# Performance work log

Hardware: AMD Instinct MI355X
Metric: run time of the kernel (lower is better)

## Reference

```python
import jax, jax.numpy as jnp
import numpy as np

B, L, D = 8, 4096, 512  # batch, seq_len (power of 2), in_features
R_MIN, R_MAX = 0.9, 0.999


def setup_inputs() -> dict:
    key = jax.random.key(0)
    k1, k2, k3 = jax.random.split(key, 3)
    inputs = jax.random.normal(k1, (B, L, D), dtype=jnp.float32)
    # Linear layers: i_dense D->2D, o_dense 2D->D (torch Linear: y = x @ W.T + b)
    Wi = jax.random.normal(k2, (2 * D, D), dtype=jnp.float32) / np.sqrt(D)
    bi = jnp.zeros((2 * D,), dtype=jnp.float32)
    Wo = jax.random.normal(k3, (D, 2 * D), dtype=jnp.float32) / np.sqrt(2 * D)
    bo = jnp.zeros((D,), dtype=jnp.float32)
    # LRU param init, exactly as in the torch module
    rng = np.random.RandomState(0)
    u1 = rng.random_sample(D)
    u2 = rng.random_sample(D)
    v_log = np.log(-0.5 * np.log(u1 * (R_MAX ** 2 - R_MIN ** 2) + R_MIN ** 2))
    theta_log = np.log(u2 * np.pi * 2)
    gamma_log = np.log(np.sqrt(1 - np.exp(-np.exp(v_log)) ** 2))
    params_log = jnp.asarray(np.stack([v_log, theta_log, gamma_log]), dtype=jnp.float32)
    return {"inputs": inputs, "Wi": Wi, "bi": bi, "Wo": Wo, "bo": bo,
            "params_log": params_log}


def reference(inputs, Wi, bi, Wo, bo, params_log):
    b, lin, d = inputs.shape
    u = inputs @ Wi.T + bi                       # [B, L, 2D]
    params = jnp.exp(params_log)                 # [3, D]
    v, theta, gamma = params[0], params[1], params[2]
    log2_L = int(np.ceil(np.log2(lin)))
    Lp = 2 ** log2_L
    # interleaved (real, imag) pairs -> complex state
    u = u.reshape(b, lin, d, 2)
    x = jax.lax.complex(u[..., 0], u[..., 1])    # [B, L, D] complex64
    if Lp > lin:
        x = jnp.pad(x, ((0, 0), (0, Lp - lin), (0, 0)))
    # Blelloch-style doubling scan: after stage i, each block of length 2^i
    # holds the prefix-scanned values x_t = lam*x_{t-1} + u_t within the block.
    for i in range(1, log2_L + 1):
        l = 2 ** i
        xr = x.reshape(b * Lp // l, l, d)
        x1, x2 = xr[:, : l // 2], xr[:, l // 2 :]
        pos = jnp.arange(1, l // 2 + 1, dtype=jnp.float32)        # [l/2]
        lambs = jnp.exp(jax.lax.complex(-pos[:, None] * v,
                                        pos[:, None] * theta))   # [l/2, D]
        x2 = x2 + lambs * x1[:, -1:]
        x = jnp.concatenate([x1, x2], axis=1).reshape(b, Lp, d)
    x = x[:, :lin] * gamma.astype(jnp.complex64)
    xr = jnp.concatenate([jnp.real(x), jnp.imag(x)], axis=-1)     # [B, L, 2D]
    out = xr @ Wo.T + bo
    return jax.nn.relu(out)
```

## Files before the change

kernel.cpp:

```cpp
#include <hip/hip_runtime.h>
#include <cstdint>
#include <cstddef>

typedef unsigned short u16;
typedef unsigned int   u32;

typedef short bf16x8 __attribute__((ext_vector_type(8)));
typedef float f32x4  __attribute__((ext_vector_type(4)));

__device__ __forceinline__ u16 f2bf(float f) {
  u32 u = __float_as_uint(f);
  u += 0x7fffu + ((u >> 16) & 1u);
  return (u16)(u >> 16);
}
__device__ __forceinline__ float bflo(u32 w) { return __uint_as_float((w & 0xffffu) << 16); }
__device__ __forceinline__ float bfhi(u32 w) { return __uint_as_float(w & 0xffff0000u); }

#define GLB_AS(p) ((const __attribute__((address_space(1))) void*)(p))
#define LDS_AS(p) ((__attribute__((address_space(3))) void*)(p))

__global__ __launch_bounds__(256)
void conv3_f32_bf16(const float* __restrict__ in, u16* __restrict__ a,
                    const float* __restrict__ wi, u16* __restrict__ wib,
                    const float* __restrict__ wo, u16* __restrict__ wob)
{
  long i = (long)blockIdx.x * 256 + threadIdx.x;
  const float* src; u16* dst;
  if (i < 4194304L) { src = in; dst = a; }
  else if (i < 4325376L) { i -= 4194304L; src = wi; dst = wib; }
  else { i -= 4325376L; if (i >= 131072L) return; src = wo; dst = wob; }
  float4 v = ((const float4*)src)[i];
  u32 lo = (u32)f2bf(v.x) | ((u32)f2bf(v.y) << 16);
  u32 hi = (u32)f2bf(v.z) | ((u32)f2bf(v.w) << 16);
  ((uint2*)dst)[i] = make_uint2(lo, hi);
}

template<int N, int K, int LOGNB, int OUT_BF16, int RELU>
__global__ __launch_bounds__(512, 4)
void gemm_w2(const u16* __restrict__ A, const u16* __restrict__ Bw,
             const float* __restrict__ bias, void* __restrict__ Cout)
{
  __shared__ __align__(16) u16 As[256 * 32];
  __shared__ __align__(16) u16 Bs[128 * 32];

  const int tid  = threadIdx.x;
  const int lane = tid & 63;
  const int wave = tid >> 6;
  const int bid  = blockIdx.x;
  const int xcd  = bid & 7;
  const int s    = bid >> 3;
  const int m0 = (xcd * 16 + (s >> LOGNB)) * 256;
  const int n0 = (s & ((1 << LOGNB) - 1)) * 128;
  const int wm = (wave & 3) * 64;
  const int wn = (wave >> 2) * 64;

  f32x4 acc[4][4];
#pragma unroll
  for (int i = 0; i < 4; ++i)
#pragma unroll
    for (int j = 0; j < 4; ++j) acc[i][j] = f32x4{0.f, 0.f, 0.f, 0.f};

  const u16* Ap[2]; const u16* Bp; int ldsA[2]; int ldsB;
#pragma unroll
  for (int i = 0; i < 2; ++i) {
    int g = i * 512 + tid;
    int r = g >> 2;
    int koff = ((g & 3) ^ ((r >> 1) & 3)) << 3;
    Ap[i]   = A + (size_t)(m0 + r) * K + koff;
    ldsA[i] = (i * 512 + wave * 64) * 8;
  }
  {
    int g = tid;
    int r = g >> 2;
    int koff = ((g & 3) ^ ((r >> 1) & 3)) << 3;
    Bp   = Bw + (size_t)(n0 + r) * K + koff;
    ldsB = (wave * 64) * 8;
  }

  const int fm = lane & 15;
  const int q  = lane >> 4;
  int aoff[4], boff[4];
#pragma unroll
  for (int i = 0; i < 4; ++i) {
    int m = wm + i * 16 + fm;
    aoff[i] = (m * 4 + (q ^ ((m >> 1) & 3))) * 8;
    int n = wn + i * 16 + fm;
    boff[i] = (n * 4 + (q ^ ((n >> 1) & 3))) * 8;
  }

  for (int kt = 0; kt < K; kt += 32) {
    __builtin_amdgcn_global_load_lds(GLB_AS(Ap[0] + kt), LDS_AS(As + ldsA[0]), 16, 0, 0);
    __builtin_amdgcn_global_load_lds(GLB_AS(Ap[1] + kt), LDS_AS(As + ldsA[1]), 16, 0, 0);
    __builtin_amdgcn_global_load_lds(GLB_AS(Bp    + kt), LDS_AS(Bs + ldsB),    16, 0, 0);
    __syncthreads();

    bf16x8 af[4], bf[4];
#pragma unroll
    for (int i = 0; i < 4; ++i) { af[i] = *(const bf16x8*)&As[aoff[i]];
                                  bf[i] = *(const bf16x8*)&Bs[boff[i]]; }
#pragma unroll
    for (int mi = 0; mi < 4; ++mi)
#pragma unroll
      for (int ni = 0; ni < 4; ++ni)
        acc[mi][ni] = __builtin_amdgcn_mfma_f32_16x16x32_bf16(af[mi], bf[ni],
                                                              acc[mi][ni], 0, 0, 0);
    __syncthreads();
  }

  const int colL = lane & 15;
  const int rowQ = (lane >> 4) * 4;
#pragma unroll
  for (int mi = 0; mi < 4; ++mi) {
#pragma unroll
    for (int ni = 0; ni < 4; ++ni) {
      int col  = n0 + wn + ni * 16 + colL;
      int rowb = m0 + wm + mi * 16 + rowQ;
      float bv = bias[col];
#pragma unroll
      for (int r = 0; r < 4; ++r) {
        float v = acc[mi][ni][r] + bv;
        if (RELU) v = fmaxf(v, 0.f);
        size_t idx = (size_t)(rowb + r) * N + col;
        if (OUT_BF16) ((u16*)Cout)[idx] = f2bf(v);
        else          ((float*)Cout)[idx] = v;
      }
    }
  }
}

__global__ __launch_bounds__(256)
void scan_chunk_end(const u16* __restrict__ u, const float* __restrict__ plog,
                    float2* __restrict__ e)
{
  const int t = threadIdx.x;
  const int c = blockIdx.x;
  const int b = blockIdx.y;
  const int j0 = 2 * t;
  float v0 = expf(plog[j0]),        v1 = expf(plog[j0 + 1]);
  float t0 = expf(plog[512 + j0]),  t1 = expf(plog[512 + j0 + 1]);
  float m0 = expf(-v0), m1 = expf(-v1);
  float lr0 = m0 * cosf(t0), li0 = m0 * sinf(t0);
  float lr1 = m1 * cosf(t1), li1 = m1 * sinf(t1);
  const uint2* up = (const uint2*)u;
  size_t idx = (size_t)(b * 4096 + c * 32) * 256 + t;
  float h0r = 0.f, h0i = 0.f, h1r = 0.f, h1i = 0.f;
#pragma unroll 8
  for (int s = 0; s < 32; ++s) {
    uint2 w = up[idx]; idx += 256;
    float u0r = bflo(w.x), u0i = bfhi(w.x);
    float u1r = bflo(w.y), u1i = bfhi(w.y);
    float n0r = fmaf(lr0, h0r, fmaf(-li0, h0i, u0r));
    float n0i = fmaf(lr0, h0i, fmaf( li0, h0r, u0i));
    float n1r = fmaf(lr1, h1r, fmaf(-li1, h1i, u1r));
    float n1i = fmaf(lr1, h1i, fmaf( li1, h1r, u1i));
    h0r = n0r; h0i = n0i; h1r = n1r; h1i = n1i;
  }
  ((float4*)e)[(size_t)(b * 128 + c) * 256 + t] = make_float4(h0r, h0i, h1r, h1i);
}

__global__ __launch_bounds__(256)
void scan_out2(const u16* __restrict__ u, const float* __restrict__ plog,
               const float2* __restrict__ e, u16* __restrict__ xr)
{
  const int t = threadIdx.x;
  const int c = blockIdx.x;
  const int b = blockIdx.y;
  const int j0 = 2 * t;
  float v0 = expf(plog[j0]),        v1 = expf(plog[j0 + 1]);
  float t0 = expf(plog[512 + j0]),  t1 = expf(plog[512 + j0 + 1]);
  float g0 = expf(plog[1024 + j0]), g1 = expf(plog[1024 + j0 + 1]);
  float m0 = expf(-v0), m1 = expf(-v1);
  float lr0 = m0 * cosf(t0), li0 = m0 * sinf(t0);
  float lr1 = m1 * cosf(t1), li1 = m1 * sinf(t1);

  float Lm0 = expf(-32.f * v0), Lm1 = expf(-32.f * v1);
  float La0 = 32.f * t0,        La1 = 32.f * t1;
  float Lr0 = Lm0 * cosf(La0), Li0 = Lm0 * sinf(La0);
  float Lr1 = Lm1 * cosf(La1), Li1 = Lm1 * sinf(La1);
  float h0r = 0.f, h0i = 0.f, h1r = 0.f, h1i = 0.f;
  const float4* e4 = (const float4*)e;
#pragma unroll 4
  for (int i = 0; i < c; ++i) {
    float4 ec = e4[(size_t)(b * 128 + i) * 256 + t];
    float n0r = fmaf(Lr0, h0r, fmaf(-Li0, h0i, ec.x));
    float n0i = fmaf(Lr0, h0i, fmaf( Li0, h0r, ec.y));
    float n1r = fmaf(Lr1, h1r, fmaf(-Li1, h1i, ec.z));
    float n1i = fmaf(Lr1, h1i, fmaf( Li1, h1r, ec.w));
    h0r = n0r; h0i = n0i; h1r = n1r; h1i = n1i;
  }

  const uint2* up = (const uint2*)u;
  u32* xp = (u32*)xr;
  size_t uidx = (size_t)(b * 4096 + c * 32) * 256 + t;
  size_t xidx = (size_t)(b * 4096 + c * 32) * 512 + t;
#pragma unroll 8
  for (int s = 0; s < 32; ++s) {
    uint2 w = up[uidx]; uidx += 256;
    float u0r = bflo(w.x), u0i = bfhi(w.x);
    float u1r = bflo(w.y), u1i = bfhi(w.y);
    float n0r = fmaf(lr0, h0r, fmaf(-li0, h0i, u0r));
    float n0i = fmaf(lr0, h0i, fmaf( li0, h0r, u0i));
    float n1r = fmaf(lr1, h1r, fmaf(-li1, h1i, u1r));
    float n1i = fmaf(lr1, h1i, fmaf( li1, h1r, u1i));
    h0r = n0r; h0i = n0i; h1r = n1r; h1i = n1i;
    xp[xidx]       = (u32)f2bf(g0 * h0r) | ((u32)f2bf(g1 * h1r) << 16);
    xp[xidx + 256] = (u32)f2bf(g0 * h0i) | ((u32)f2bf(g1 * h1i) << 16);
    xidx += 512;
  }
}

extern "C" void kernel_launch(void* const* d_in, const int* in_sizes, int n_in,
                              void* d_out, int out_size, void* d_ws, size_t ws_size,
                              hipStream_t stream)
{
  (void)in_sizes; (void)n_in; (void)out_size; (void)ws_size;
  const float* inputs = (const float*)d_in[0];
  const float* Wi     = (const float*)d_in[1];
  const float* bi     = (const float*)d_in[2];
  const float* Wo     = (const float*)d_in[3];
  const float* bo     = (const float*)d_in[4];
  const float* plog   = (const float*)d_in[5];

  char* ws = (char*)d_ws;
  u16*    xrA   = (u16*)(ws);
  u16*    u_bf  = (u16*)(ws + 67108864ull);
  u16*    Wi_bf = (u16*)(ws + 134217728ull);
  u16*    Wo_bf = (u16*)(ws + 135266304ull);
  float2* e_b   = (float2*)(ws + 136314880ull);

  conv3_f32_bf16<<<17408, 256, 0, stream>>>(inputs, xrA, Wi, Wi_bf, Wo, Wo_bf);

  gemm_w2<1024, 512, 3, 1, 0><<<1024, 512, 0, stream>>>(xrA, Wi_bf, bi, u_bf);

  scan_chunk_end<<<dim3(128, 8), 256, 0, stream>>>(u_bf, plog, e_b);
  scan_out2<<<dim3(128, 8), 256, 0, stream>>>(u_bf, plog, e_b, xrA);

  gemm_w2<512, 1024, 2, 0, 1><<<512, 512, 0, stream>>>(xrA, Wo_bf, bo, d_out);
}
```

Before: 258.6 us.

## Triple-buffer GEMM LDS loads and add a separate chunk-carry scan kernel

The GEMM main loop now uses three LDS buffers with global_load_lds prefetch two tiles ahead, so the second barrier per k-step goes away and loads overlap the MFMA work. The scan's cross-chunk carry moves into a new 8-block kernel that sequentially propagates the chunk-end states in place. Before, each scan_out2 block re-scanned every earlier chunk, which is quadratic redundant work. The plog parameter loads are also vectorized. Costs are triple the GEMM LDS footprint, which may lower occupancy, plus an extra serial, low-parallelism kernel launch.

After: 252.5 us. -2.4%, faster.

```diff
diff --git a/kernel.cpp b/kernel.cpp
--- a/kernel.cpp
+++ b/kernel.cpp
@@ -40,8 +40,8 @@
 void gemm_w2(const u16* __restrict__ A, const u16* __restrict__ Bw,
              const float* __restrict__ bias, void* __restrict__ Cout)
 {
-  __shared__ __align__(16) u16 As[256 * 32];
-  __shared__ __align__(16) u16 Bs[128 * 32];
+  __shared__ __align__(16) u16 As[3][256 * 32];
+  __shared__ __align__(16) u16 Bs[3][128 * 32];
 
   const int tid  = threadIdx.x;
   const int lane = tid & 63;
@@ -88,24 +88,37 @@
     boff[i] = (n * 4 + (q ^ ((n >> 1) & 3))) * 8;
   }
 
-  for (int kt = 0; kt < K; kt += 32) {
-    __builtin_amdgcn_global_load_lds(GLB_AS(Ap[0] + kt), LDS_AS(As + ldsA[0]), 16, 0, 0);
-    __builtin_amdgcn_global_load_lds(GLB_AS(Ap[1] + kt), LDS_AS(As + ldsA[1]), 16, 0, 0);
-    __builtin_amdgcn_global_load_lds(GLB_AS(Bp    + kt), LDS_AS(Bs + ldsB),    16, 0, 0);
-    __syncthreads();
-
-    bf16x8 af[4], bf[4];
-#pragma unroll
-    for (int i = 0; i < 4; ++i) { af[i] = *(const bf16x8*)&As[aoff[i]];
-                                  bf[i] = *(const bf16x8*)&Bs[boff[i]]; }
+  auto stage = [&](int buf, int kt) {
+    __builtin_amdgcn_global_load_lds(GLB_AS(Ap[0] + kt), LDS_AS(&As[buf][ldsA[0]]), 16, 0, 0);
+    __builtin_amdgcn_global_load_lds(GLB_AS(Ap[1] + kt), LDS_AS(&As[buf][ldsA[1]]), 16, 0, 0);
+    __builtin_amdgcn_global_load_lds(GLB_AS(Bp    + kt), LDS_AS(&Bs[buf][ldsB]),    16, 0, 0);
+  };
+  auto compute = [&](int buf) {
+    bf16x8 af[4], bfr[4];
+#pragma unroll
+    for (int i = 0; i < 4; ++i) { af[i]  = *(const bf16x8*)&As[buf][aoff[i]];
+                                  bfr[i] = *(const bf16x8*)&Bs[buf][boff[i]]; }
 #pragma unroll
     for (int mi = 0; mi < 4; ++mi)
 #pragma unroll
       for (int ni = 0; ni < 4; ++ni)
-        acc[mi][ni] = __builtin_amdgcn_mfma_f32_16x16x32_bf16(af[mi], bf[ni],
+        acc[mi][ni] = __builtin_amdgcn_mfma_f32_16x16x32_bf16(af[mi], bfr[ni],
                                                               acc[mi][ni], 0, 0, 0);
-    __syncthreads();
-  }
+  };
+
+  constexpr int NT = K / 32;
+  stage(0, 0);
+  stage(1, 32);
+#pragma unroll
+  for (int t = 0; t < NT - 1; ++t) {
+    asm volatile("s_waitcnt vmcnt(3)" ::: "memory");
+    __builtin_amdgcn_s_barrier();
+    if (t + 2 < NT) stage((t + 2) % 3, (t + 2) * 32);
+    compute(t % 3);
+  }
+  asm volatile("s_waitcnt vmcnt(0)" ::: "memory");
+  __builtin_amdgcn_s_barrier();
+  compute((NT - 1) % 3);
 
   const int colL = lane & 15;
   const int rowQ = (lane >> 4) * 4;
@@ -135,9 +148,10 @@
   const int t = threadIdx.x;
   const int c = blockIdx.x;
   const int b = blockIdx.y;
-  const int j0 = 2 * t;
-  float v0 = expf(plog[j0]),        v1 = expf(plog[j0 + 1]);
-  float t0 = expf(plog[512 + j0]),  t1 = expf(plog[512 + j0 + 1]);
+  float2 vl = ((const float2*)plog)[t];
+  float2 tl = ((const float2*)plog)[256 + t];
+  float v0 = expf(vl.x), v1 = expf(vl.y);
+  float t0 = expf(tl.x), t1 = expf(tl.y);
   float m0 = expf(-v0), m1 = expf(-v1);
   float lr0 = m0 * cosf(t0), li0 = m0 * sinf(t0);
   float lr1 = m1 * cosf(t1), li1 = m1 * sinf(t1);
@@ -159,34 +173,53 @@
 }
 
 __global__ __launch_bounds__(256)
-void scan_out2(const u16* __restrict__ u, const float* __restrict__ plog,
-               const float2* __restrict__ e, u16* __restrict__ xr)
+void scan_mid(const float* __restrict__ plog, float4* __restrict__ e)
 {
   const int t = threadIdx.x;
-  const int c = blockIdx.x;
-  const int b = blockIdx.y;
-  const int j0 = 2 * t;
-  float v0 = expf(plog[j0]),        v1 = expf(plog[j0 + 1]);
-  float t0 = expf(plog[512 + j0]),  t1 = expf(plog[512 + j0 + 1]);
-  float g0 = expf(plog[1024 + j0]), g1 = expf(plog[1024 + j0 + 1]);
-  float m0 = expf(-v0), m1 = expf(-v1);
-  float lr0 = m0 * cosf(t0), li0 = m0 * sinf(t0);
-  float lr1 = m1 * cosf(t1), li1 = m1 * sinf(t1);
-
+  const int b = blockIdx.x;
+  float2 vl = ((const float2*)plog)[t];
+  float2 tl = ((const float2*)plog)[256 + t];
+  float v0 = expf(vl.x), v1 = expf(vl.y);
+  float t0 = expf(tl.x), t1 = expf(tl.y);
   float Lm0 = expf(-32.f * v0), Lm1 = expf(-32.f * v1);
   float La0 = 32.f * t0,        La1 = 32.f * t1;
   float Lr0 = Lm0 * cosf(La0), Li0 = Lm0 * sinf(La0);
   float Lr1 = Lm1 * cosf(La1), Li1 = Lm1 * sinf(La1);
   float h0r = 0.f, h0i = 0.f, h1r = 0.f, h1i = 0.f;
-  const float4* e4 = (const float4*)e;
+  size_t base = (size_t)(b * 128) * 256 + t;
 #pragma unroll 4
-  for (int i = 0; i < c; ++i) {
-    float4 ec = e4[(size_t)(b * 128 + i) * 256 + t];
+  for (int c = 0; c < 128; ++c) {
+    float4 ec = e[base + (size_t)c * 256];
     float n0r = fmaf(Lr0, h0r, fmaf(-Li0, h0i, ec.x));
     float n0i = fmaf(Lr0, h0i, fmaf( Li0, h0r, ec.y));
     float n1r = fmaf(Lr1, h1r, fmaf(-Li1, h1i, ec.z));
     float n1i = fmaf(Lr1, h1i, fmaf( Li1, h1r, ec.w));
     h0r = n0r; h0i = n0i; h1r = n1r; h1i = n1i;
+    e[base + (size_t)c * 256] = make_float4(h0r, h0i, h1r, h1i);
+  }
+}
+
+__global__ __launch_bounds__(256)
+void scan_out2(const u16* __restrict__ u, const float* __restrict__ plog,
+               const float4* __restrict__ e, u16* __restrict__ xr)
+{
+  const int t = threadIdx.x;
+  const int c = blockIdx.x;
+  const int b = blockIdx.y;
+  float2 vl = ((const float2*)plog)[t];
+  float2 tl = ((const float2*)plog)[256 + t];
+  float2 gl = ((const float2*)plog)[512 + t];
+  float v0 = expf(vl.x), v1 = expf(vl.y);
+  float t0 = expf(tl.x), t1 = expf(tl.y);
+  float g0 = expf(gl.x), g1 = expf(gl.y);
+  float m0 = expf(-v0), m1 = expf(-v1);
+  float lr0 = m0 * cosf(t0), li0 = m0 * sinf(t0);
+  float lr1 = m1 * cosf(t1), li1 = m1 * sinf(t1);
+
+  float h0r = 0.f, h0i = 0.f, h1r = 0.f, h1i = 0.f;
+  if (c > 0) {
+    float4 ec = e[(size_t)(b * 128 + c - 1) * 256 + t];
+    h0r = ec.x; h0i = ec.y; h1r = ec.z; h1i = ec.w;
   }
 
   const uint2* up = (const uint2*)u;
@@ -233,7 +266,8 @@
   gemm_w2<1024, 512, 3, 1, 0><<<1024, 512, 0, stream>>>(xrA, Wi_bf, bi, u_bf);
 
   scan_chunk_end<<<dim3(128, 8), 256, 0, stream>>>(u_bf, plog, e_b);
-  scan_out2<<<dim3(128, 8), 256, 0, stream>>>(u_bf, plog, e_b, xrA);
+  scan_mid<<<8, 256, 0, stream>>>(plog, (float4*)e_b);
+  scan_out2<<<dim3(128, 8), 256, 0, stream>>>(u_bf, plog, (const float4*)e_b, xrA);
 
   gemm_w2<512, 1024, 2, 0, 1><<<512, 512, 0, stream>>>(xrA, Wo_bf, bo, d_out);
 }
```
